# Optimization experiments

Hardware: AMD Instinct MI355X
Metric: run time of the kernel (lower is better)

## Reference

```python
import jax, jax.numpy as jnp
import numpy as np

N_NODES = 100000
N_EDGES = 3200000
F_IN, H_ENC, H_GCN, H_Q, A_DIM = 128, 128, 128, 256, 10


def setup_inputs() -> dict:
    key = jax.random.key(0)
    ks = jax.random.split(key, 8)
    s = lambda d: 1.0 / np.sqrt(d)
    return {
        "x": jax.random.normal(ks[0], (N_NODES, F_IN), jnp.float32),
        "edge_index": jax.random.randint(ks[1], (2, N_EDGES), 0, N_NODES, jnp.int64),
        "W_enc": jax.random.normal(ks[2], (F_IN, H_ENC), jnp.float32) * s(F_IN),
        "b_enc": jnp.zeros((H_ENC,), jnp.float32),
        "W_gcn": jax.random.normal(ks[3], (H_ENC, H_GCN), jnp.float32) * s(H_ENC),
        "b_gcn": jnp.zeros((H_GCN,), jnp.float32),
        "W1": jax.random.normal(ks[4], (H_GCN, H_Q), jnp.float32) * s(H_GCN),
        "b1": jnp.zeros((H_Q,), jnp.float32),
        "W2": jax.random.normal(ks[5], (H_Q, A_DIM), jnp.float32) * s(H_Q),
        "b2": jnp.zeros((A_DIM,), jnp.float32),
    }


def gcn_conv(x, edge_index, W, b):
    # Standard GCNConv: D^{-1/2} (A + I) D^{-1/2} X W + b, symmetric norm with self-loops.
    n = x.shape[0]
    src, dst = edge_index[0], edge_index[1]
    xw = x @ W  # [N, H]
    deg = jnp.ones((n,), xw.dtype).at[dst].add(1.0)  # in-degree + self-loop
    dinv = jax.lax.rsqrt(deg)
    coef = dinv[src] * dinv[dst]  # [E]
    msg = xw[src] * coef[:, None]  # [E, H] gather-scale
    agg = jax.ops.segment_sum(msg, dst, num_segments=n)  # scatter-add
    agg = agg + xw * (dinv * dinv)[:, None]  # self-loop contribution
    return agg + b


def reference(x, edge_index, W_enc, b_enc, W_gcn, b_gcn, W1, b1, W2, b2):
    h = jax.nn.relu(x @ W_enc + b_enc)              # Encoder: Linear + ReLU
    h = jax.nn.relu(gcn_conv(h, edge_index, W_gcn, b_gcn))  # GCNConv + ReLU
    q = jax.nn.relu(h @ W1 + b1) @ W2 + b2          # Q_Net MLP
    return q
```

## Files before the change

kernel.cpp:

```cpp
#include <hip/hip_runtime.h>

#define N_NODES 100000
constexpr int F     = 128;
constexpr int NB    = (N_NODES + 63) / 64;
constexpr int BCAP  = 2496;
constexpr int LCAP  = 80;
constexpr int CHUNK = 8192;
constexpr int EPT   = CHUNK / 512;
constexpr int PADN  = N_NODES;

typedef __attribute__((ext_vector_type(8))) short short8;
typedef __attribute__((ext_vector_type(4))) float f32x4;
typedef __attribute__((ext_vector_type(4))) short short4v;
typedef __attribute__((ext_vector_type(4))) unsigned uint4v;

__device__ inline short f2bf(float v) {
    union { float f; unsigned u; } x; x.f = v;
    unsigned r = (x.u + 0x7fff + ((x.u >> 16) & 1)) >> 16;
    return (short)r;
}
__device__ inline float lo_bf(unsigned v) {
    union { unsigned u; float f; } x; x.u = v << 16; return x.f;
}
__device__ inline float hi_bf(unsigned v) {
    union { unsigned u; float f; } x; x.u = v & 0xffff0000u; return x.f;
}

__global__ __launch_bounds__(256) void prep_kernel(const float* __restrict__ W_enc,
                                                   const float* __restrict__ W_gcn,
                                                   const float* __restrict__ W1,
                                                   const float* __restrict__ W2,
                                                   short* __restrict__ Wte,
                                                   short* __restrict__ Wtg,
                                                   short* __restrict__ Wt1,
                                                   short* __restrict__ W2t) {
    int idx = blockIdx.x * 256 + threadIdx.x;
    if (idx < 16384) { int h = idx >> 7, k = idx & 127; Wte[idx] = f2bf(W_enc[k * 128 + h]); return; }
    idx -= 16384;
    if (idx < 16384) { int h = idx >> 7, k = idx & 127; Wtg[idx] = f2bf(W_gcn[k * 128 + h]); return; }
    idx -= 16384;
    if (idx < 32768) { int h = idx >> 7, k = idx & 127; Wt1[idx] = f2bf(W1[k * 256 + h]); return; }
    idx -= 32768;
    if (idx < 4096)  { int n = idx >> 8, k = idx & 255; W2t[idx] = (n < 10) ? f2bf(W2[k * 10 + n]) : (short)0; }
}

__global__ __launch_bounds__(512, 4) void part_kernel(const int* __restrict__ src,
                                                      const int* __restrict__ dst,
                                                      int* __restrict__ bcur,
                                                      int* __restrict__ part, int E) {
    __shared__ int cnt[NB];
    __shared__ int base[NB];
    for (int b = threadIdx.x; b < NB; b += 512) cnt[b] = 0;
    __syncthreads();
    const int e0 = blockIdx.x * CHUNK;
    const int e1 = min(e0 + CHUNK, E);

    int pk[EPT];
    int meta[EPT];
#pragma unroll
    for (int i = 0; i < EPT; ++i) {
        int e = e0 + i * 512 + (int)threadIdx.x;
        meta[i] = -1;
        if (e < e1) {
            int d = dst[e];
            int b = d >> 6;
            pk[i] = src[e] | ((d & 63) << 17);
            int pos = atomicAdd(&cnt[b], 1);
            meta[i] = b | (pos << 11);
        }
    }
    __syncthreads();
    for (int b = threadIdx.x; b < NB; b += 512) {
        int c = cnt[b];
        base[b] = c ? atomicAdd(&bcur[b], c) : 0;
    }
    __syncthreads();
#pragma unroll
    for (int i = 0; i < EPT; ++i) {
        if (meta[i] >= 0) {
            int b = meta[i] & 0x7FF;
            int idx = base[b] + (meta[i] >> 11);
            if (idx < BCAP) part[b * BCAP + idx] = pk[i];
        }
    }
}

__global__ __launch_bounds__(256) void deg_kernel(const int* __restrict__ bcur,
                                                  const int* __restrict__ part,
                                                  float* __restrict__ dinv) {
    __shared__ int deg_l[64];
    const int b = blockIdx.x;
    if (threadIdx.x < 64) deg_l[threadIdx.x] = 0;
    __syncthreads();
    const int cnt = min(bcur[b], BCAP);
    const int* p = part + (size_t)b * BCAP;
#pragma unroll 4
    for (int i = threadIdx.x; i < cnt; i += 256)
        atomicAdd(&deg_l[(p[i] >> 17) & 63], 1);
    __syncthreads();
    if (threadIdx.x < 64)
        dinv[b * 64 + threadIdx.x] = rsqrtf(1.f + (float)deg_l[threadIdx.x]);
}

__global__ __launch_bounds__(256) void gemmA_kernel(const float* __restrict__ x,
                                                    const short* __restrict__ Wte,
                                                    const short* __restrict__ Wtg,
                                                    const float* __restrict__ b_enc,
                                                    const float* __restrict__ dinv,
                                                    short* __restrict__ xs) {
    __shared__ short h_l[4][16][136];
    const int b = blockIdx.x;
    const int wave = threadIdx.x >> 6;
    const int lane = threadIdx.x & 63;
    const int quad = lane >> 4;
    const int l16  = lane & 15;
    const int node0 = b * 64 + wave * 16;
    int nrow = node0 + l16;
    const bool valid = nrow < N_NODES;
    if (!valid) nrow = N_NODES - 1;

    const float dvn = dinv[nrow];

    f32x4 acc[8] = {};
#pragma unroll
    for (int kc = 0; kc < 4; ++kc) {
        const float* ap = x + (size_t)nrow * 128 + kc * 32 + quad * 8;
        float4 f0 = *reinterpret_cast<const float4*>(ap);
        float4 f1 = *reinterpret_cast<const float4*>(ap + 4);
        short8 xfrag;
        xfrag.s0 = f2bf(f0.x); xfrag.s1 = f2bf(f0.y); xfrag.s2 = f2bf(f0.z); xfrag.s3 = f2bf(f0.w);
        xfrag.s4 = f2bf(f1.x); xfrag.s5 = f2bf(f1.y); xfrag.s6 = f2bf(f1.z); xfrag.s7 = f2bf(f1.w);
#pragma unroll
        for (int t = 0; t < 8; ++t) {
            short8 wfrag = *reinterpret_cast<const short8*>(Wte + (size_t)(t * 16 + l16) * 128 + kc * 32 + quad * 8);
            acc[t] = __builtin_amdgcn_mfma_f32_16x16x32_bf16(wfrag, xfrag, acc[t], 0, 0, 0);
        }
    }
#pragma unroll
    for (int t = 0; t < 8; ++t) {
        short4v o;
#pragma unroll
        for (int r = 0; r < 4; ++r)
            ((short*)&o)[r] = f2bf(fmaxf(acc[t][r] + b_enc[t * 16 + quad * 4 + r], 0.f));
        *reinterpret_cast<short4v*>(&h_l[wave][l16][t * 16 + quad * 4]) = o;
    }

    f32x4 acc2[8] = {};
#pragma unroll
    for (int kc = 0; kc < 4; ++kc) {
        short8 xfrag = *reinterpret_cast<const short8*>(&h_l[wave][l16][kc * 32 + quad * 8]);
#pragma unroll
        for (int t = 0; t < 8; ++t) {
            short8 wfrag = *reinterpret_cast<const short8*>(Wtg + (size_t)(t * 16 + l16) * 128 + kc * 32 + quad * 8);
            acc2[t] = __builtin_amdgcn_mfma_f32_16x16x32_bf16(wfrag, xfrag, acc2[t], 0, 0, 0);
        }
    }
    const int srow = node0 + l16;
#pragma unroll
    for (int t = 0; t < 8; ++t) {
        short4v o;
#pragma unroll
        for (int r = 0; r < 4; ++r)
            ((short*)&o)[r] = valid ? f2bf(acc2[t][r] * dvn) : (short)0;
        *reinterpret_cast<short4v*>(xs + (size_t)srow * 128 + t * 16 + quad * 4) = o;
    }
}

__global__ __launch_bounds__(512, 8) void agg_kernel(const short* __restrict__ xs,
                                                     const int* __restrict__ bcur,
                                                     const int* __restrict__ part,
                                                     const float* __restrict__ bg,
                                                     short* __restrict__ h2) {
    __shared__ int csr_l[64 * LCAP];
    __shared__ int cur[64];
    const int b = blockIdx.x;
    const int tid = threadIdx.x;
    if (tid < 64) cur[tid] = 0;
    __syncthreads();
    const int cnt = min(bcur[b], BCAP);
    const int* p = part + (size_t)b * BCAP;
#pragma unroll 4
    for (int i = tid; i < cnt; i += 512) {
        int v = p[i];
        int ld = (v >> 17) & 63;
        int pos = atomicAdd(&cur[ld], 1);
        if (pos < LCAP) csr_l[ld * LCAP + pos] = v & 0x1FFFF;
    }
    __syncthreads();
    if (tid < 64) {
        int d = min(cur[tid], LCAP);
        int dp = (d + 15) & ~15;
        for (int k = d; k < dp; ++k) csr_l[tid * LCAP + k] = PADN;
    }
    __syncthreads();

    const int wave = tid >> 6;
    const int lane = tid & 63;
    const int g    = lane >> 4;
    const int l16  = lane & 15;
    const uint4v* xs4 = reinterpret_cast<const uint4v*>(xs);
    const float4 bgA = reinterpret_cast<const float4*>(bg)[l16 * 2];
    const float4 bgB = reinterpret_cast<const float4*>(bg)[l16 * 2 + 1];

    for (int t = 0; t < 8; ++t) {
        const int ld = wave * 8 + t;
        const int node = b * 64 + ld;
        if (node >= N_NODES) break;

        const int dtrue = cur[ld];
        const int dpad = (min(dtrue, LCAP) + 15) & ~15;
        const float dv = rsqrtf(1.f + (float)dtrue);
        const int* cl = csr_l + ld * LCAP;

        float a0 = 0.f, a1 = 0.f, a2 = 0.f, a3 = 0.f, a4 = 0.f, a5 = 0.f, a6 = 0.f, a7 = 0.f;
        for (int j = 0; j < dpad; j += 16) {
            int s[4];
            uint4v v[4];
#pragma unroll
            for (int u = 0; u < 4; ++u) s[u] = cl[j + u * 4 + g];
#pragma unroll
            for (int u = 0; u < 4; ++u) v[u] = xs4[((size_t)s[u] << 4) + l16];
#pragma unroll
            for (int u = 0; u < 4; ++u) {
                a0 += lo_bf(v[u].x); a1 += hi_bf(v[u].x);
                a2 += lo_bf(v[u].y); a3 += hi_bf(v[u].y);
                a4 += lo_bf(v[u].z); a5 += hi_bf(v[u].z);
                a6 += lo_bf(v[u].w); a7 += hi_bf(v[u].w);
            }
        }
        a0 += __shfl_xor(a0, 16, 64); a0 += __shfl_xor(a0, 32, 64);
        a1 += __shfl_xor(a1, 16, 64); a1 += __shfl_xor(a1, 32, 64);
        a2 += __shfl_xor(a2, 16, 64); a2 += __shfl_xor(a2, 32, 64);
        a3 += __shfl_xor(a3, 16, 64); a3 += __shfl_xor(a3, 32, 64);
        a4 += __shfl_xor(a4, 16, 64); a4 += __shfl_xor(a4, 32, 64);
        a5 += __shfl_xor(a5, 16, 64); a5 += __shfl_xor(a5, 32, 64);
        a6 += __shfl_xor(a6, 16, 64); a6 += __shfl_xor(a6, 32, 64);
        a7 += __shfl_xor(a7, 16, 64); a7 += __shfl_xor(a7, 32, 64);
        if (g == 0) {
            uint4v vs = xs4[((size_t)node << 4) + l16];
            a0 += lo_bf(vs.x); a1 += hi_bf(vs.x);
            a2 += lo_bf(vs.y); a3 += hi_bf(vs.y);
            a4 += lo_bf(vs.z); a5 += hi_bf(vs.z);
            a6 += lo_bf(vs.w); a7 += hi_bf(vs.w);
            short8 o;
            o.s0 = f2bf(fmaxf(fmaf(a0, dv, bgA.x), 0.f));
            o.s1 = f2bf(fmaxf(fmaf(a1, dv, bgA.y), 0.f));
            o.s2 = f2bf(fmaxf(fmaf(a2, dv, bgA.z), 0.f));
            o.s3 = f2bf(fmaxf(fmaf(a3, dv, bgA.w), 0.f));
            o.s4 = f2bf(fmaxf(fmaf(a4, dv, bgB.x), 0.f));
            o.s5 = f2bf(fmaxf(fmaf(a5, dv, bgB.y), 0.f));
            o.s6 = f2bf(fmaxf(fmaf(a6, dv, bgB.z), 0.f));
            o.s7 = f2bf(fmaxf(fmaf(a7, dv, bgB.w), 0.f));
            *reinterpret_cast<short8*>(h2 + ((size_t)node << 7) + l16 * 8) = o;
        }
    }
}

__global__ __launch_bounds__(256) void gemmB_kernel(const short* __restrict__ h2,
                                                    const short* __restrict__ Wt1,
                                                    const short* __restrict__ W2t,
                                                    const float* __restrict__ b1,
                                                    const float* __restrict__ b2,
                                                    float* __restrict__ q) {
    __shared__ short hq_l[4][16][264];
    const int wave = threadIdx.x >> 6;
    const int lane = threadIdx.x & 63;
    const int quad = lane >> 4;
    const int l16  = lane & 15;
    const int node0 = blockIdx.x * 128 + wave * 32;

    int r0 = node0 + l16;
    int r1 = node0 + 16 + l16;
    if (r0 >= N_NODES) r0 = N_NODES - 1;
    if (r1 >= N_NODES) r1 = N_NODES - 1;

    f32x4 acc0[16] = {}, acc1[16] = {};
#pragma unroll
    for (int kc = 0; kc < 4; ++kc) {
        short8 xf0 = *reinterpret_cast<const short8*>(h2 + (size_t)r0 * 128 + kc * 32 + quad * 8);
        short8 xf1 = *reinterpret_cast<const short8*>(h2 + (size_t)r1 * 128 + kc * 32 + quad * 8);
#pragma unroll
        for (int t = 0; t < 16; ++t) {
            short8 wfrag = *reinterpret_cast<const short8*>(Wt1 + (size_t)(t * 16 + l16) * 128 + kc * 32 + quad * 8);
            acc0[t] = __builtin_amdgcn_mfma_f32_16x16x32_bf16(wfrag, xf0, acc0[t], 0, 0, 0);
            acc1[t] = __builtin_amdgcn_mfma_f32_16x16x32_bf16(wfrag, xf1, acc1[t], 0, 0, 0);
        }
    }

#pragma unroll
    for (int half = 0; half < 2; ++half) {
        const f32x4* acc = half ? acc1 : acc0;
        const int nb = node0 + half * 16;
#pragma unroll
        for (int t = 0; t < 16; ++t) {
            short4v o;
#pragma unroll
            for (int r = 0; r < 4; ++r)
                ((short*)&o)[r] = f2bf(fmaxf(acc[t][r] + b1[t * 16 + quad * 4 + r], 0.f));
            *reinterpret_cast<short4v*>(&hq_l[wave][l16][t * 16 + quad * 4]) = o;
        }

        f32x4 a2 = {};
#pragma unroll
        for (int kc = 0; kc < 8; ++kc) {
            short8 afrag = *reinterpret_cast<const short8*>(&hq_l[wave][l16][kc * 32 + quad * 8]);
            short8 bfrag = *reinterpret_cast<const short8*>(W2t + (size_t)l16 * 256 + kc * 32 + quad * 8);
            a2 = __builtin_amdgcn_mfma_f32_16x16x32_bf16(afrag, bfrag, a2, 0, 0, 0);
        }
        if (l16 < 10) {
            float bv = b2[l16];
#pragma unroll
            for (int r = 0; r < 4; ++r) {
                int nd = nb + quad * 4 + r;
                if (nd < N_NODES) q[(size_t)nd * 10 + l16] = a2[r] + bv;
            }
        }
    }
}

extern "C" void kernel_launch(void* const* d_in, const int* in_sizes, int n_in,
                              void* d_out, int out_size, void* d_ws, size_t ws_size,
                              hipStream_t stream) {
    const float* x     = (const float*)d_in[0];
    const int*   ei    = (const int*)d_in[1];
    const float* W_enc = (const float*)d_in[2];
    const float* b_enc = (const float*)d_in[3];
    const float* W_gcn = (const float*)d_in[4];
    const float* b_gcn = (const float*)d_in[5];
    const float* W1    = (const float*)d_in[6];
    const float* b1    = (const float*)d_in[7];
    const float* W2    = (const float*)d_in[8];
    const float* b2    = (const float*)d_in[9];
    float* q = (float*)d_out;

    const int E = in_sizes[1] / 2;
    const int* srcv = ei;
    const int* dstv = ei + E;

    char* ws = (char*)d_ws;
    const size_t XSB = (size_t)(NB * 64) * 128 * sizeof(short);
    short* xs  = (short*)(ws);
    short* h2  = (short*)(ws + XSB);
    int*   part= (int*)  (ws + 2 * XSB);
    char*  tail = ws + 2 * XSB + (size_t)NB * BCAP * sizeof(int);
    int*   bcr = (int*)(tail);
    float* dinv= (float*)(tail + 8192);
    short* Wte = (short*)(tail + 408576);
    short* Wtg = (short*)(tail + 441344);
    short* Wt1 = (short*)(tail + 474112);
    short* W2t = (short*)(tail + 539648);

    hipMemsetAsync(bcr, 0, 8192, stream);
    prep_kernel<<<272, 256, 0, stream>>>(W_enc, W_gcn, W1, W2, Wte, Wtg, Wt1, W2t);
    part_kernel<<<(E + CHUNK - 1) / CHUNK, 512, 0, stream>>>(srcv, dstv, bcr, part, E);
    deg_kernel<<<NB, 256, 0, stream>>>(bcr, part, dinv);
    gemmA_kernel<<<NB, 256, 0, stream>>>(x, Wte, Wtg, b_enc, dinv, xs);
    agg_kernel<<<NB, 512, 0, stream>>>(xs, bcr, part, b_gcn, h2);
    gemmB_kernel<<<(N_NODES + 127) / 128, 256, 0, stream>>>(h2, Wt1, W2t, b1, b2, q);
}
```

Baseline: 389.8 us.

## Split aggregation feature dimension across two blocks, use dot2 bf16 accumulate, fold memset

Each 64-node aggregation bucket is now handled by two blocks, each gathering half of the 128 features (8-byte loads instead of 16-byte), which doubles block count for more parallelism and latency hiding. The bf16-to-f32 unpack and add is replaced by v_dot2_f32_bf16 against mask constants, so each instruction extracts and accumulates one element in one step. The bucket-counter memset is folded into prep_kernel to remove a separate launch. The cost is that each block rebuilds the local CSR from the partition, so that work is done twice, and each gathered row segment is narrower.

```diff
diff --git a/kernel.cpp b/kernel.cpp
--- a/kernel.cpp
+++ b/kernel.cpp
@@ -19,11 +19,10 @@
     unsigned r = (x.u + 0x7fff + ((x.u >> 16) & 1)) >> 16;
     return (short)r;
 }
-__device__ inline float lo_bf(unsigned v) {
-    union { unsigned u; float f; } x; x.u = v << 16; return x.f;
-}
-__device__ inline float hi_bf(unsigned v) {
-    union { unsigned u; float f; } x; x.u = v & 0xffff0000u; return x.f;
+
+__device__ inline void dot2acc(float& alo, float& ahi, unsigned w, unsigned mlo, unsigned mhi) {
+    asm("v_dot2_f32_bf16 %0, %1, %2, %0" : "+v"(alo) : "v"(w), "v"(mlo));
+    asm("v_dot2_f32_bf16 %0, %1, %2, %0" : "+v"(ahi) : "v"(w), "v"(mhi));
 }
 
 __global__ __launch_bounds__(256) void prep_kernel(const float* __restrict__ W_enc,
@@ -33,7 +32,8 @@
                                                    short* __restrict__ Wte,
                                                    short* __restrict__ Wtg,
                                                    short* __restrict__ Wt1,
-                                                   short* __restrict__ W2t) {
+                                                   short* __restrict__ W2t,
+                                                   int* __restrict__ bcr) {
     int idx = blockIdx.x * 256 + threadIdx.x;
     if (idx < 16384) { int h = idx >> 7, k = idx & 127; Wte[idx] = f2bf(W_enc[k * 128 + h]); return; }
     idx -= 16384;
@@ -41,7 +41,9 @@
     idx -= 16384;
     if (idx < 32768) { int h = idx >> 7, k = idx & 127; Wt1[idx] = f2bf(W1[k * 256 + h]); return; }
     idx -= 32768;
-    if (idx < 4096)  { int n = idx >> 8, k = idx & 255; W2t[idx] = (n < 10) ? f2bf(W2[k * 10 + n]) : (short)0; }
+    if (idx < 4096)  { int n = idx >> 8, k = idx & 255; W2t[idx] = (n < 10) ? f2bf(W2[k * 10 + n]) : (short)0; return; }
+    idx -= 4096;
+    if (idx < NB) bcr[idx] = 0;
 }
 
 __global__ __launch_bounds__(512, 4) void part_kernel(const int* __restrict__ src,
@@ -173,7 +175,8 @@
                                                      short* __restrict__ h2) {
     __shared__ int csr_l[64 * LCAP];
     __shared__ int cur[64];
-    const int b = blockIdx.x;
+    const int b    = blockIdx.x >> 1;
+    const int half = blockIdx.x & 1;
     const int tid = threadIdx.x;
     if (tid < 64) cur[tid] = 0;
     __syncthreads();
@@ -198,9 +201,11 @@
     const int lane = tid & 63;
     const int g    = lane >> 4;
     const int l16  = lane & 15;
-    const uint4v* xs4 = reinterpret_cast<const uint4v*>(xs);
-    const float4 bgA = reinterpret_cast<const float4*>(bg)[l16 * 2];
-    const float4 bgB = reinterpret_cast<const float4*>(bg)[l16 * 2 + 1];
+    const uint2* xs2 = reinterpret_cast<const uint2*>(xs);
+    const int fo = half * 16 + l16;
+    const float4 bgv = reinterpret_cast<const float4*>(bg)[fo];
+    unsigned mlo = 0x00003F80u;
+    unsigned mhi = 0x3F800000u;
 
     for (int t = 0; t < 8; ++t) {
         const int ld = wave * 8 + t;
@@ -212,46 +217,34 @@
         const float dv = rsqrtf(1.f + (float)dtrue);
         const int* cl = csr_l + ld * LCAP;
 
-        float a0 = 0.f, a1 = 0.f, a2 = 0.f, a3 = 0.f, a4 = 0.f, a5 = 0.f, a6 = 0.f, a7 = 0.f;
+        float a0 = 0.f, a1 = 0.f, a2 = 0.f, a3 = 0.f;
         for (int j = 0; j < dpad; j += 16) {
             int s[4];
-            uint4v v[4];
+            uint2 v[4];
 #pragma unroll
             for (int u = 0; u < 4; ++u) s[u] = cl[j + u * 4 + g];
 #pragma unroll
-            for (int u = 0; u < 4; ++u) v[u] = xs4[((size_t)s[u] << 4) + l16];
+            for (int u = 0; u < 4; ++u) v[u] = xs2[(size_t)s[u] * 32 + fo];
 #pragma unroll
             for (int u = 0; u < 4; ++u) {
-                a0 += lo_bf(v[u].x); a1 += hi_bf(v[u].x);
-                a2 += lo_bf(v[u].y); a3 += hi_bf(v[u].y);
-                a4 += lo_bf(v[u].z); a5 += hi_bf(v[u].z);
-                a6 += lo_bf(v[u].w); a7 += hi_bf(v[u].w);
+                dot2acc(a0, a1, v[u].x, mlo, mhi);
+                dot2acc(a2, a3, v[u].y, mlo, mhi);
             }
         }
         a0 += __shfl_xor(a0, 16, 64); a0 += __shfl_xor(a0, 32, 64);
         a1 += __shfl_xor(a1, 16, 64); a1 += __shfl_xor(a1, 32, 64);
         a2 += __shfl_xor(a2, 16, 64); a2 += __shfl_xor(a2, 32, 64);
         a3 += __shfl_xor(a3, 16, 64); a3 += __shfl_xor(a3, 32, 64);
-        a4 += __shfl_xor(a4, 16, 64); a4 += __shfl_xor(a4, 32, 64);
-        a5 += __shfl_xor(a5, 16, 64); a5 += __shfl_xor(a5, 32, 64);
-        a6 += __shfl_xor(a6, 16, 64); a6 += __shfl_xor(a6, 32, 64);
-        a7 += __shfl_xor(a7, 16, 64); a7 += __shfl_xor(a7, 32, 64);
         if (g == 0) {
-            uint4v vs = xs4[((size_t)node << 4) + l16];
-            a0 += lo_bf(vs.x); a1 += hi_bf(vs.x);
-            a2 += lo_bf(vs.y); a3 += hi_bf(vs.y);
-            a4 += lo_bf(vs.z); a5 += hi_bf(vs.z);
-            a6 += lo_bf(vs.w); a7 += hi_bf(vs.w);
-            short8 o;
-            o.s0 = f2bf(fmaxf(fmaf(a0, dv, bgA.x), 0.f));
-            o.s1 = f2bf(fmaxf(fmaf(a1, dv, bgA.y), 0.f));
-            o.s2 = f2bf(fmaxf(fmaf(a2, dv, bgA.z), 0.f));
-            o.s3 = f2bf(fmaxf(fmaf(a3, dv, bgA.w), 0.f));
-            o.s4 = f2bf(fmaxf(fmaf(a4, dv, bgB.x), 0.f));
-            o.s5 = f2bf(fmaxf(fmaf(a5, dv, bgB.y), 0.f));
-            o.s6 = f2bf(fmaxf(fmaf(a6, dv, bgB.z), 0.f));
-            o.s7 = f2bf(fmaxf(fmaf(a7, dv, bgB.w), 0.f));
-            *reinterpret_cast<short8*>(h2 + ((size_t)node << 7) + l16 * 8) = o;
+            uint2 vs = xs2[(size_t)node * 32 + fo];
+            dot2acc(a0, a1, vs.x, mlo, mhi);
+            dot2acc(a2, a3, vs.y, mlo, mhi);
+            short4v o;
+            ((short*)&o)[0] = f2bf(fmaxf(fmaf(a0, dv, bgv.x), 0.f));
+            ((short*)&o)[1] = f2bf(fmaxf(fmaf(a1, dv, bgv.y), 0.f));
+            ((short*)&o)[2] = f2bf(fmaxf(fmaf(a2, dv, bgv.z), 0.f));
+            ((short*)&o)[3] = f2bf(fmaxf(fmaf(a3, dv, bgv.w), 0.f));
+            *reinterpret_cast<short4v*>(h2 + ((size_t)node << 7) + fo * 4) = o;
         }
     }
 }
@@ -350,11 +343,10 @@
     short* Wt1 = (short*)(tail + 474112);
     short* W2t = (short*)(tail + 539648);
 
-    hipMemsetAsync(bcr, 0, 8192, stream);
-    prep_kernel<<<272, 256, 0, stream>>>(W_enc, W_gcn, W1, W2, Wte, Wtg, Wt1, W2t);
+    prep_kernel<<<279, 256, 0, stream>>>(W_enc, W_gcn, W1, W2, Wte, Wtg, Wt1, W2t, bcr);
     part_kernel<<<(E + CHUNK - 1) / CHUNK, 512, 0, stream>>>(srcv, dstv, bcr, part, E);
     deg_kernel<<<NB, 256, 0, stream>>>(bcr, part, dinv);
     gemmA_kernel<<<NB, 256, 0, stream>>>(x, Wte, Wtg, b_enc, dinv, xs);
-    agg_kernel<<<NB, 512, 0, stream>>>(xs, bcr, part, b_gcn, h2);
+    agg_kernel<<<2 * NB, 512, 0, stream>>>(xs, bcr, part, b_gcn, h2);
     gemmB_kernel<<<(N_NODES + 127) / 128, 256, 0, stream>>>(h2, Wt1, W2t, b1, b2, q);
 }
```

Measured after the change: 377.3 us. 3.2% less time.
